# Performance work log

Measured on AMD Instinct MI355X. Metric: run time of the kernel, lower is better.

The kernel has to match this reference:

```python
import jax, jax.numpy as jnp
import numpy as np

N_HEAD = 16
N_EMBD = 1024
HEAD_DIM = N_EMBD // N_HEAD


def setup_inputs() -> dict:
    key = jax.random.key(0)
    k1, k2, k3 = jax.random.split(key, 3)
    B, T, C = 2, 2048, N_EMBD
    x = jax.random.normal(k1, (B, T, C), dtype=jnp.float32)
    # nn.Linear weights: (out_features, in_features)
    W_attn = jax.random.normal(k2, (3 * C, C), dtype=jnp.float32) * 0.02
    W_proj = jax.random.normal(k3, (C, C), dtype=jnp.float32) * 0.02
    return {"x": x, "W_attn": W_attn, "W_proj": W_proj}


def reference(x, W_attn, W_proj):
    B, T, C = x.shape
    h, hd = N_HEAD, HEAD_DIM
    # c_attn: x @ W^T, then split into q, k, v
    qkv = jnp.einsum('btc,dc->btd', x, W_attn)  # [B, T, 3C]
    q, k, v = jnp.split(qkv, 3, axis=-1)
    # [B, T, C] -> [B, h, T, hd]
    q = q.reshape(B, T, h, hd).transpose(0, 2, 1, 3)
    k = k.reshape(B, T, h, hd).transpose(0, 2, 1, 3)
    v = v.reshape(B, T, h, hd).transpose(0, 2, 1, 3)
    # NOTE: no 1/sqrt(hd) scaling in the original module
    logits = jnp.einsum('bhnk,bhmk->bhnm', q, k)  # [B, h, T, T]
    causal = jnp.tril(jnp.ones((T, T), dtype=bool))  # [T, T]
    logits = jnp.where(causal[None, None, :, :], logits, -jnp.inf)
    weights = jax.nn.softmax(logits, axis=-1)
    O = jnp.einsum('bhnm,bhmv->bhnv', weights, v)  # [B, h, T, hd]
    # Original: einsum('bhnv,hdv->bnd', O, c_proj.weight) with weight viewed as (h, d, v)
    Wp = W_proj.reshape(h, C, hd)
    Y = jnp.einsum('bhnv,hdv->bnd', O, Wp)  # [B, T, C]
    return Y
```

## Files before the change

kernel.cpp:

```cpp
#include <hip/hip_runtime.h>
#include <stdint.h>
#include <math.h>

#define B_    2
#define T_    2048
#define C_    1024
#define H_    16
#define D_    64
#define MTOT  4096
#define NQKV  3072
#define KDIM  1024

#define LOG2E 1.4426950408889634f

typedef short short8 __attribute__((ext_vector_type(8)));
typedef float f32x4  __attribute__((ext_vector_type(4)));

__device__ __forceinline__ uint16_t f2b(float f) {
    union { float f; uint32_t u; } x; x.f = f;
    uint32_t u = x.u;
    return (uint16_t)((u + 0x7FFFu + ((u >> 16) & 1u)) >> 16);
}
__device__ __forceinline__ uint32_t packb2(float a, float b) {
    union { float f; uint32_t u; } x, y; x.f = a; y.f = b;
    return ((x.u + 0x8000u) >> 16) | ((y.u + 0x8000u) & 0xffff0000u);
}
__device__ __forceinline__ uint32_t packb2_rne(float a, float b) {
    return (uint32_t)f2b(a) | ((uint32_t)f2b(b) << 16);
}
__device__ __forceinline__ float fexp2(float x) {
#if __has_builtin(__builtin_amdgcn_exp2f)
    return __builtin_amdgcn_exp2f(x);
#else
    return exp2f(x);
#endif
}

__global__ __launch_bounds__(256) void cast_all(const float* __restrict__ x,
                                                const float* __restrict__ wa,
                                                uint16_t* __restrict__ xb,
                                                uint16_t* __restrict__ wab,
                                                int n4x, int n4w) {
    int i = blockIdx.x * blockDim.x + threadIdx.x;
    const float* src; uint16_t* dst; int j;
    if (i < n4x) { src = x; dst = xb; j = i; }
    else { j = i - n4x; if (j >= n4w) return; src = wa; dst = wab; }
    float4 v = ((const float4*)src)[j];
    ushort4 o;
    o.x = f2b(v.x); o.y = f2b(v.y); o.z = f2b(v.z); o.w = f2b(v.w);
    ((ushort4*)dst)[j] = o;
}

__global__ __launch_bounds__(256) void cast_wp(const float* __restrict__ wp,
                                               uint16_t* __restrict__ wt) {
    int i = blockIdx.x * blockDim.x + threadIdx.x;
    int j4 = (i & 255) * 4;
    int d  = i >> 8;
    int h = j4 >> 6, v = j4 & 63;
    float4 val = *(const float4*)(wp + h * 65536 + d * 64 + v);
    ushort4 o;
    o.x = f2b(val.x); o.y = f2b(val.y); o.z = f2b(val.z); o.w = f2b(val.w);
    *(ushort4*)(wt + d * 1024 + j4) = o;
}

__global__ __launch_bounds__(256, 3) void gemm_qkv(const uint16_t* __restrict__ A,
                                                   const uint16_t* __restrict__ Bw,
                                                   uint16_t* __restrict__ qkvb) {
    __shared__ __align__(16) uint16_t As[128 * 64];
    __shared__ __align__(16) uint16_t Bs[128 * 64];

    int tid = threadIdx.x;
    int w = tid >> 6, lane = tid & 63;
    int qd = lane >> 4, ln = lane & 15;
    int lnx = ln & 7;
    int rowBase = blockIdx.y * 128;
    int colBase = blockIdx.x * 128;
    int mw = (w >> 1) * 64, nw = (w & 1) * 64;

    int srow = tid >> 3;
    int pchunk = tid & 7;
    int gchunk = pchunk ^ (srow & 7);

    const uint16_t* ga = A  + (size_t)(rowBase + srow) * KDIM + gchunk * 8;
    const uint16_t* gb = Bw + (size_t)(colBase + srow) * KDIM + gchunk * 8;
    uint16_t* la = &As[srow * 64 + pchunk * 8];
    uint16_t* lb = &Bs[srow * 64 + pchunk * 8];

    short8 paE[4], paO[4], pb[4];
#pragma unroll
    for (int m = 0; m < 4; m++) {
        paE[m] = *(const short8*)(ga + (size_t)m * 32 * KDIM);
        paO[m] = *(const short8*)(ga + 64 + (size_t)m * 32 * KDIM);
        pb[m]  = *(const short8*)(gb + (size_t)m * 32 * KDIM);
    }

    f32x4 acc[4][4] = {};

#define QSTEP(PAC, S)                                                            \
    {                                                                            \
        _Pragma("unroll")                                                        \
        for (int m = 0; m < 4; m++) {                                            \
            *(short8*)(la + m * 32 * 64) = PAC[m];                               \
            *(short8*)(lb + m * 32 * 64) = pb[m];                                \
        }                                                                        \
        __syncthreads();                                                         \
        if ((S) + 1 < 16) {                                                      \
            int kb_ = ((S) + 1) * 64;                                            \
            _Pragma("unroll")                                                    \
            for (int m = 0; m < 4; m++)                                          \
                pb[m] = *(const short8*)(gb + kb_ + (size_t)m * 32 * KDIM);      \
        }                                                                        \
        if ((S) + 2 < 16) {                                                      \
            int ka_ = ((S) + 2) * 64;                                            \
            _Pragma("unroll")                                                    \
            for (int m = 0; m < 4; m++)                                          \
                PAC[m] = *(const short8*)(ga + ka_ + (size_t)m * 32 * KDIM);     \
        }                                                                        \
        _Pragma("unroll")                                                        \
        for (int ks = 0; ks < 2; ks++) {                                         \
            int p = (ks * 4 + qd) ^ lnx;                                         \
            short8 a_[4], b_[4];                                                 \
            _Pragma("unroll")                                                    \
            for (int i = 0; i < 4; i++) {                                        \
                a_[i] = *(const short8*)&As[(mw + i * 16 + ln) * 64 + p * 8];    \
                b_[i] = *(const short8*)&Bs[(nw + i * 16 + ln) * 64 + p * 8];    \
            }                                                                    \
            _Pragma("unroll")                                                    \
            for (int i = 0; i < 4; i++)                                          \
                _Pragma("unroll")                                                \
                for (int j = 0; j < 4; j++)                                      \
                    acc[i][j] = __builtin_amdgcn_mfma_f32_16x16x32_bf16(a_[i], b_[j], acc[i][j], 0, 0, 0); \
        }                                                                        \
        __syncthreads();                                                         \
    }

    for (int sp = 0; sp < 8; sp++) {
        QSTEP(paE, 2 * sp);
        QSTEP(paO, 2 * sp + 1);
    }
#undef QSTEP

#pragma unroll
    for (int i = 0; i < 4; i++) {
#pragma unroll
        for (int j = 0; j < 4; j++) {
            int gcol = colBase + nw + j * 16 + ln;
            int which = gcol >> 10;
            int rem = gcol & 1023;
            int h = rem >> 6, d = rem & 63;
            if (which == 2) {
                int t0 = rowBase + mw + i * 16 + qd * 4;
                int bb = t0 >> 11, t = t0 & 2047;
                uint2 pk2;
                pk2.x = packb2_rne(acc[i][j][0], acc[i][j][1]);
                pk2.y = packb2_rne(acc[i][j][2], acc[i][j][3]);
                *(uint2*)&qkvb[(size_t)2 * 4194304 + (((size_t)(bb * H_ + h) * D_) + d) * T_ + t] = pk2;
            } else {
                float sc = (which == 0) ? LOG2E : 1.0f;
#pragma unroll
                for (int r = 0; r < 4; r++) {
                    int grow = rowBase + mw + i * 16 + qd * 4 + r;
                    int bb = grow >> 11, t = grow & 2047;
                    uint16_t val = f2b(acc[i][j][r] * sc);
                    qkvb[(size_t)which * 4194304 + (((size_t)(bb * H_ + h) * T_) + t) * D_ + d] = val;
                }
            }
        }
    }
}


#define STRIP(QS, BQ, OT, LSUM)                                              \
    if (kt * 64 <= (QS) + 15) {                                              \
        bool needm = (kt * 64 + 63 > (QS));                                  \
        f32x4 stt[4];                                                        \
        __builtin_amdgcn_s_setprio(1);                                       \
        _Pragma("unroll")                                                    \
        for (int it = 0; it < 4; it++) {                                     \
            f32x4 z = {};                                                    \
            z = __builtin_amdgcn_mfma_f32_16x16x32_bf16(ak[it][0], (BQ)[0], z, 0, 0, 0); \
            z = __builtin_amdgcn_mfma_f32_16x16x32_bf16(ak[it][1], (BQ)[1], z, 0, 0, 0); \
            stt[it] = z;                                                     \
        }                                                                    \
        __builtin_amdgcn_s_setprio(0);                                       \
        if (needm) {                                                         \
            _Pragma("unroll")                                                \
            for (int it = 0; it < 4; it++)                                   \
                _Pragma("unroll")                                            \
                for (int r = 0; r < 4; r++) {                                \
                    int t = kt * 64 + it * 16 + qd * 4 + r;                  \
                    if (t > (QS) + ln) stt[it][r] = -1.0e30f;                \
                }                                                            \
        }                                                                    \
        _Pragma("unroll")                                                    \
        for (int it = 0; it < 4; it++) {                                     \
            float p0 = fexp2(stt[it][0]);                                    \
            float p1 = fexp2(stt[it][1]);                                    \
            float p2 = fexp2(stt[it][2]);                                    \
            float p3 = fexp2(stt[it][3]);                                    \
            (LSUM) += (p0 + p1) + (p2 + p3);                                 \
            uint2 pk2;                                                       \
            pk2.x = packb2(p0, p1);                                          \
            pk2.y = packb2(p2, p3);                                          \
            *(uint2*)&Pl[w][ln][it * 16 + qd * 4] = pk2;                     \
        }                                                                    \
        short8 bp0 = *(const short8*)&Pl[w][ln][qd * 8];                     \
        short8 bp1 = *(const short8*)&Pl[w][ln][32 + qd * 8];                \
        __builtin_amdgcn_s_setprio(1);                                       \
        _Pragma("unroll")                                                    \
        for (int id = 0; id < 4; id++) {                                     \
            (OT)[id] = __builtin_amdgcn_mfma_f32_16x16x32_bf16(av[id][0], bp0, (OT)[id], 0, 0, 0); \
            (OT)[id] = __builtin_amdgcn_mfma_f32_16x16x32_bf16(av[id][1], bp1, (OT)[id], 0, 0, 0); \
        }                                                                    \
        __builtin_amdgcn_s_setprio(0);                                       \
    }

#define EPI(QS, OT, LSUM)                                                    \
    {                                                                        \
        float ssum = (LSUM);                                                 \
        ssum += __shfl_xor(ssum, 16);                                        \
        ssum += __shfl_xor(ssum, 32);                                        \
        float rl = 1.0f / ssum;                                              \
        int q = (QS) + ln;                                                   \
        _Pragma("unroll")                                                    \
        for (int id = 0; id < 4; id++) {                                     \
            float v0 = (OT)[id][0] * rl;                                     \
            float v1 = (OT)[id][1] * rl;                                     \
            float v2 = (OT)[id][2] * rl;                                     \
            float v3 = (OT)[id][3] * rl;                                     \
            uint2 pk2;                                                       \
            pk2.x = packb2_rne(v0, v1);                                      \
            pk2.y = packb2_rne(v2, v3);                                      \
            *(uint2*)&oc[(size_t)(b * T_ + q) * C_ + h * 64 + id * 16 + qd * 4] = pk2; \
        }                                                                    \
    }

__global__ __launch_bounds__(512, 2) void attn(const uint16_t* __restrict__ qkvb,
                                               uint16_t* __restrict__ oc) {
    __shared__ __align__(16) uint16_t Ks[2][64 * 64];
    __shared__ __align__(16) uint16_t Vs[2][64 * 64];
    __shared__ __align__(16) uint16_t Pl[8][16][72];

    int tid = threadIdx.x;
    int w = tid >> 6, lane = tid & 63;
    int qd = lane >> 4, ln = lane & 15;
    int lnx = ln & 7;
    int bid = blockIdx.x;
    int j = bid >> 5;
    int bh = bid & 31;
    int b = bh >> 4, h = bh & 15;

    const uint16_t* Q0 = qkvb + (size_t)bh * T_ * D_;
    const uint16_t* K  = Q0 + 4194304;
    const uint16_t* Vt = qkvb + (size_t)2 * 4194304 + (size_t)bh * D_ * T_;

    int qsA = j * 128 + w * 16;
    int qsB = (15 - j) * 128 + w * 16;
    int nt  = 32 - 2 * j;

    short8 bqA[2], bqB[2];
#pragma unroll
    for (int ks = 0; ks < 2; ks++) {
        bqA[ks] = *(const short8*)(Q0 + (size_t)(qsA + ln) * D_ + ks * 32 + qd * 8);
        bqB[ks] = *(const short8*)(Q0 + (size_t)(qsB + ln) * D_ + ks * 32 + qd * 8);
    }

    int srow = tid >> 3;
    int pch = tid & 7;
    int gch = pch ^ (srow & 7);
    const uint16_t* gk = K  + (size_t)srow * D_ + gch * 8;
    const uint16_t* gv = Vt + (size_t)srow * T_ + gch * 8;
    int lofs = srow * 64 + pch * 8;

    short8 pk = *(const short8*)gk;
    short8 pv = *(const short8*)gv;

    f32x4 otA[4] = {}, otB[4] = {};
    float lA = 0.f, lB = 0.f;

    int c = 0;
    for (int kt = 0; kt < nt; kt++) {
        *(short8*)&Ks[c][lofs] = pk;
        *(short8*)&Vs[c][lofs] = pv;
        __syncthreads();
        if (kt + 1 < nt) {
            pk = *(const short8*)(gk + (size_t)(kt + 1) * 64 * D_);
            pv = *(const short8*)(gv + (size_t)(kt + 1) * 64);
        }
        short8 ak[4][2], av[4][2];
#pragma unroll
        for (int ks = 0; ks < 2; ks++) {
            int p8 = ((ks * 4 + qd) ^ lnx) * 8;
#pragma unroll
            for (int it = 0; it < 4; it++) {
                ak[it][ks] = *(const short8*)&Ks[c][(it * 16 + ln) * 64 + p8];
                av[it][ks] = *(const short8*)&Vs[c][(it * 16 + ln) * 64 + p8];
            }
        }
        STRIP(qsA, bqA, otA, lA);
        STRIP(qsB, bqB, otB, lB);
        c ^= 1;
    }

    EPI(qsA, otA, lA);
    EPI(qsB, otB, lB);
}

__global__ __launch_bounds__(256, 3) void gemm_out(const uint16_t* __restrict__ A,
                                                   const uint16_t* __restrict__ Bw,
                                                   float* __restrict__ out) {
    __shared__ __align__(16) uint16_t As[128 * 64];
    __shared__ __align__(16) uint16_t Bs[64 * 64];

    int tid = threadIdx.x;
    int w = tid >> 6, lane = tid & 63;
    int qd = lane >> 4, ln = lane & 15;
    int lnx = ln & 7;
    int rowBase = blockIdx.y * 128;
    int colBase = blockIdx.x * 64;
    int mw = (w >> 1) * 64, nw = (w & 1) * 32;

    int srow = tid >> 3;
    int pchunk = tid & 7;
    int gchunk = pchunk ^ (srow & 7);

    const uint16_t* ga = A  + (size_t)(rowBase + srow) * KDIM + gchunk * 8;
    const uint16_t* gb = Bw + (size_t)(colBase + srow) * KDIM + gchunk * 8;
    uint16_t* la = &As[srow * 64 + pchunk * 8];
    uint16_t* lb = &Bs[srow * 64 + pchunk * 8];

    short8 paE[4], paO[4], pb[2];
#pragma unroll
    for (int m = 0; m < 4; m++) {
        paE[m] = *(const short8*)(ga + (size_t)m * 32 * KDIM);
        paO[m] = *(const short8*)(ga + 64 + (size_t)m * 32 * KDIM);
    }
#pragma unroll
    for (int m = 0; m < 2; m++)
        pb[m] = *(const short8*)(gb + (size_t)m * 32 * KDIM);

    f32x4 acc[4][2] = {};

#define OSTEP(PAC, S)                                                            \
    {                                                                            \
        _Pragma("unroll")                                                        \
        for (int m = 0; m < 4; m++)                                              \
            *(short8*)(la + m * 32 * 64) = PAC[m];                               \
        _Pragma("unroll")                                                        \
        for (int m = 0; m < 2; m++)                                              \
            *(short8*)(lb + m * 32 * 64) = pb[m];                                \
        __syncthreads();                                                         \
        if ((S) + 1 < 16) {                                                      \
            int kb_ = ((S) + 1) * 64;                                            \
            _Pragma("unroll")                                                    \
            for (int m = 0; m < 2; m++)                                          \
                pb[m] = *(const short8*)(gb + kb_ + (size_t)m * 32 * KDIM);      \
        }                                                                        \
        if ((S) + 2 < 16) {                                                      \
            int ka_ = ((S) + 2) * 64;                                            \
            _Pragma("unroll")                                                    \
            for (int m = 0; m < 4; m++)                                          \
                PAC[m] = *(const short8*)(ga + ka_ + (size_t)m * 32 * KDIM);     \
        }                                                                        \
        _Pragma("unroll")                                                        \
        for (int ks = 0; ks < 2; ks++) {                                         \
            int p = (ks * 4 + qd) ^ lnx;                                         \
            short8 a_[4], b_[2];                                                 \
            _Pragma("unroll")                                                    \
            for (int i = 0; i < 4; i++)                                          \
                a_[i] = *(const short8*)&As[(mw + i * 16 + ln) * 64 + p * 8];    \
            _Pragma("unroll")                                                    \
            for (int j = 0; j < 2; j++)                                          \
                b_[j] = *(const short8*)&Bs[(nw + j * 16 + ln) * 64 + p * 8];    \
            _Pragma("unroll")                                                    \
            for (int i = 0; i < 4; i++)                                          \
                _Pragma("unroll")                                                \
                for (int j = 0; j < 2; j++)                                      \
                    acc[i][j] = __builtin_amdgcn_mfma_f32_16x16x32_bf16(a_[i], b_[j], acc[i][j], 0, 0, 0); \
        }                                                                        \
        __syncthreads();                                                         \
    }

    for (int sp = 0; sp < 8; sp++) {
        OSTEP(paE, 2 * sp);
        OSTEP(paO, 2 * sp + 1);
    }
#undef OSTEP

#pragma unroll
    for (int i = 0; i < 4; i++)
#pragma unroll
        for (int j = 0; j < 2; j++)
#pragma unroll
            for (int r = 0; r < 4; r++) {
                int grow = rowBase + mw + i * 16 + qd * 4 + r;
                int gcol = colBase + nw + j * 16 + ln;
                out[(size_t)grow * 1024 + gcol] = acc[i][j][r];
            }
}

extern "C" void kernel_launch(void* const* d_in, const int* in_sizes, int n_in,
                              void* d_out, int out_size, void* d_ws, size_t ws_size,
                              hipStream_t stream) {
    const float* x  = (const float*)d_in[0];
    const float* Wa = (const float*)d_in[1];
    const float* Wp = (const float*)d_in[2];
    float* out = (float*)d_out;

    uint16_t* ws   = (uint16_t*)d_ws;
    uint16_t* xb   = ws;
    uint16_t* Wab  = xb + 4194304;
    uint16_t* Wtb  = Wab + 3145728;
    uint16_t* qkvb = Wtb + 1048576;
    uint16_t* ob   = qkvb + (size_t)3 * 4194304;

    cast_all<<<7168, 256, 0, stream>>>(x, Wa, xb, Wab, 4194304 / 4, 3145728 / 4);
    cast_wp<<<1024, 256, 0, stream>>>(Wp, Wtb);
    gemm_qkv<<<dim3(24, 32), 256, 0, stream>>>(xb, Wab, qkvb);
    attn<<<256, 512, 0, stream>>>(qkvb, ob);
    gemm_out<<<dim3(16, 32), 256, 0, stream>>>(ob, Wtb, out);
}
```

Before: 164.1 us.

## Merge weight casts and split QKV GEMM into Q/K and V kernels

Folds the W_proj transpose-cast into the main cast kernel, which removes one launch. The QKV GEMM becomes two kernels. For Q/K the MFMA operands are swapped so each lane holds four consecutive head-dim values and can write packed 8-byte stores instead of scalar 2-byte scattered stores. The V kernel keeps the transposed packed store. The cost is one extra launch, a smaller grid per GEMM, and duplicated code.

```diff
diff --git a/kernel.cpp b/kernel.cpp
--- a/kernel.cpp
+++ b/kernel.cpp
@@ -36,36 +36,40 @@
 #endif
 }
 
+#define N4X 1048576
+#define N4W 786432
+#define N4P 262144
+
 __global__ __launch_bounds__(256) void cast_all(const float* __restrict__ x,
                                                 const float* __restrict__ wa,
+                                                const float* __restrict__ wp,
                                                 uint16_t* __restrict__ xb,
                                                 uint16_t* __restrict__ wab,
-                                                int n4x, int n4w) {
+                                                uint16_t* __restrict__ wt) {
     int i = blockIdx.x * blockDim.x + threadIdx.x;
-    const float* src; uint16_t* dst; int j;
-    if (i < n4x) { src = x; dst = xb; j = i; }
-    else { j = i - n4x; if (j >= n4w) return; src = wa; dst = wab; }
-    float4 v = ((const float4*)src)[j];
-    ushort4 o;
-    o.x = f2b(v.x); o.y = f2b(v.y); o.z = f2b(v.z); o.w = f2b(v.w);
-    ((ushort4*)dst)[j] = o;
-}
-
-__global__ __launch_bounds__(256) void cast_wp(const float* __restrict__ wp,
-                                               uint16_t* __restrict__ wt) {
-    int i = blockIdx.x * blockDim.x + threadIdx.x;
-    int j4 = (i & 255) * 4;
-    int d  = i >> 8;
-    int h = j4 >> 6, v = j4 & 63;
-    float4 val = *(const float4*)(wp + h * 65536 + d * 64 + v);
-    ushort4 o;
-    o.x = f2b(val.x); o.y = f2b(val.y); o.z = f2b(val.z); o.w = f2b(val.w);
-    *(ushort4*)(wt + d * 1024 + j4) = o;
-}
-
-__global__ __launch_bounds__(256, 3) void gemm_qkv(const uint16_t* __restrict__ A,
-                                                   const uint16_t* __restrict__ Bw,
-                                                   uint16_t* __restrict__ qkvb) {
+    if (i < N4X + N4W) {
+        const float* src; uint16_t* dst; int j;
+        if (i < N4X) { src = x; dst = xb; j = i; }
+        else { src = wa; dst = wab; j = i - N4X; }
+        float4 v = ((const float4*)src)[j];
+        ushort4 o;
+        o.x = f2b(v.x); o.y = f2b(v.y); o.z = f2b(v.z); o.w = f2b(v.w);
+        ((ushort4*)dst)[j] = o;
+    } else {
+        int j = i - (N4X + N4W);
+        int j4 = (j & 255) * 4;
+        int d  = j >> 8;
+        int h = j4 >> 6, v = j4 & 63;
+        float4 val = *(const float4*)(wp + h * 65536 + d * 64 + v);
+        ushort4 o;
+        o.x = f2b(val.x); o.y = f2b(val.y); o.z = f2b(val.z); o.w = f2b(val.w);
+        *(ushort4*)(wt + d * 1024 + j4) = o;
+    }
+}
+
+__global__ __launch_bounds__(256, 3) void gemm_qkv_qk(const uint16_t* __restrict__ A,
+                                                      const uint16_t* __restrict__ Bw,
+                                                      uint16_t* __restrict__ qkvb) {
     __shared__ __align__(16) uint16_t As[128 * 64];
     __shared__ __align__(16) uint16_t Bs[128 * 64];
 
@@ -129,7 +133,7 @@
             for (int i = 0; i < 4; i++)                                          \
                 _Pragma("unroll")                                                \
                 for (int j = 0; j < 4; j++)                                      \
-                    acc[i][j] = __builtin_amdgcn_mfma_f32_16x16x32_bf16(a_[i], b_[j], acc[i][j], 0, 0, 0); \
+                    acc[i][j] = __builtin_amdgcn_mfma_f32_16x16x32_bf16(b_[j], a_[i], acc[i][j], 0, 0, 0); \
         }                                                                        \
         __syncthreads();                                                         \
     }
@@ -140,31 +144,115 @@
     }
 #undef QSTEP
 
+    int which = (colBase + nw) >> 10;
+    float sc = (which == 0) ? LOG2E : 1.0f;
+#pragma unroll
+    for (int i = 0; i < 4; i++) {
+#pragma unroll
+        for (int j = 0; j < 4; j++) {
+            int mcol = colBase + nw + j * 16 + qd * 4;
+            int rem = mcol & 1023;
+            int h = rem >> 6, d0 = rem & 63;
+            int grow = rowBase + mw + i * 16 + ln;
+            int bb = grow >> 11, tt = grow & 2047;
+            uint2 pk2;
+            pk2.x = packb2_rne(acc[i][j][0] * sc, acc[i][j][1] * sc);
+            pk2.y = packb2_rne(acc[i][j][2] * sc, acc[i][j][3] * sc);
+            *(uint2*)&qkvb[(size_t)which * 4194304 + ((size_t)(bb * H_ + h) * T_ + tt) * D_ + d0] = pk2;
+        }
+    }
+}
+
+__global__ __launch_bounds__(256, 3) void gemm_qkv_v(const uint16_t* __restrict__ A,
+                                                     const uint16_t* __restrict__ Bw,
+                                                     uint16_t* __restrict__ qkvb) {
+    __shared__ __align__(16) uint16_t As[128 * 64];
+    __shared__ __align__(16) uint16_t Bs[128 * 64];
+
+    int tid = threadIdx.x;
+    int w = tid >> 6, lane = tid & 63;
+    int qd = lane >> 4, ln = lane & 15;
+    int lnx = ln & 7;
+    int rowBase = blockIdx.y * 128;
+    int colBase = 2048 + blockIdx.x * 128;
+    int mw = (w >> 1) * 64, nw = (w & 1) * 64;
+
+    int srow = tid >> 3;
+    int pchunk = tid & 7;
+    int gchunk = pchunk ^ (srow & 7);
+
+    const uint16_t* ga = A  + (size_t)(rowBase + srow) * KDIM + gchunk * 8;
+    const uint16_t* gb = Bw + (size_t)(colBase + srow) * KDIM + gchunk * 8;
+    uint16_t* la = &As[srow * 64 + pchunk * 8];
+    uint16_t* lb = &Bs[srow * 64 + pchunk * 8];
+
+    short8 paE[4], paO[4], pb[4];
+#pragma unroll
+    for (int m = 0; m < 4; m++) {
+        paE[m] = *(const short8*)(ga + (size_t)m * 32 * KDIM);
+        paO[m] = *(const short8*)(ga + 64 + (size_t)m * 32 * KDIM);
+        pb[m]  = *(const short8*)(gb + (size_t)m * 32 * KDIM);
+    }
+
+    f32x4 acc[4][4] = {};
+
+#define VSTEP(PAC, S)                                                            \
+    {                                                                            \
+        _Pragma("unroll")                                                        \
+        for (int m = 0; m < 4; m++) {                                            \
+            *(short8*)(la + m * 32 * 64) = PAC[m];                               \
+            *(short8*)(lb + m * 32 * 64) = pb[m];                                \
+        }                                                                        \
+        __syncthreads();                                                         \
+        if ((S) + 1 < 16) {                                                      \
+            int kb_ = ((S) + 1) * 64;                                            \
+            _Pragma("unroll")                                                    \
+            for (int m = 0; m < 4; m++)                                          \
+                pb[m] = *(const short8*)(gb + kb_ + (size_t)m * 32 * KDIM);      \
+        }                                                                        \
+        if ((S) + 2 < 16) {                                                      \
+            int ka_ = ((S) + 2) * 64;                                            \
+            _Pragma("unroll")                                                    \
+            for (int m = 0; m < 4; m++)                                          \
+                PAC[m] = *(const short8*)(ga + ka_ + (size_t)m * 32 * KDIM);     \
+        }                                                                        \
+        _Pragma("unroll")                                                        \
+        for (int ks = 0; ks < 2; ks++) {                                         \
+            int p = (ks * 4 + qd) ^ lnx;                                         \
+            short8 a_[4], b_[4];                                                 \
+            _Pragma("unroll")                                                    \
+            for (int i = 0; i < 4; i++) {                                        \
+                a_[i] = *(const short8*)&As[(mw + i * 16 + ln) * 64 + p * 8];    \
+                b_[i] = *(const short8*)&Bs[(nw + i * 16 + ln) * 64 + p * 8];    \
+            }                                                                    \
+            _Pragma("unroll")                                                    \
+            for (int i = 0; i < 4; i++)                                          \
+                _Pragma("unroll")                                                \
+                for (int j = 0; j < 4; j++)                                      \
+                    acc[i][j] = __builtin_amdgcn_mfma_f32_16x16x32_bf16(a_[i], b_[j], acc[i][j], 0, 0, 0); \
+        }                                                                        \
+        __syncthreads();                                                         \
+    }
+
+    for (int sp = 0; sp < 8; sp++) {
+        VSTEP(paE, 2 * sp);
+        VSTEP(paO, 2 * sp + 1);
+    }
+#undef VSTEP
+
 #pragma unroll
     for (int i = 0; i < 4; i++) {
 #pragma unroll
         for (int j = 0; j < 4; j++) {
             int gcol = colBase + nw + j * 16 + ln;
-            int which = gcol >> 10;
             int rem = gcol & 1023;
             int h = rem >> 6, d = rem & 63;
-            if (which == 2) {
-                int t0 = rowBase + mw + i * 16 + qd * 4;
-                int bb = t0 >> 11, t = t0 & 2047;
-                uint2 pk2;
-                pk2.x = packb2_rne(acc[i][j][0], acc[i][j][1]);
-                pk2.y = packb2_rne(acc[i][j][2], acc[i][j][3]);
-                *(uint2*)&qkvb[(size_t)2 * 4194304 + (((size_t)(bb * H_ + h) * D_) + d) * T_ + t] = pk2;
-            } else {
-                float sc = (which == 0) ? LOG2E : 1.0f;
-#pragma unroll
-                for (int r = 0; r < 4; r++) {
-                    int grow = rowBase + mw + i * 16 + qd * 4 + r;
-                    int bb = grow >> 11, t = grow & 2047;
-                    uint16_t val = f2b(acc[i][j][r] * sc);
-                    qkvb[(size_t)which * 4194304 + (((size_t)(bb * H_ + h) * T_) + t) * D_ + d] = val;
-                }
-            }
+            int t0 = rowBase + mw + i * 16 + qd * 4;
+            int bb = t0 >> 11, t = t0 & 2047;
+            uint2 pk2;
+            pk2.x = packb2_rne(acc[i][j][0], acc[i][j][1]);
+            pk2.y = packb2_rne(acc[i][j][2], acc[i][j][3]);
+            *(uint2*)&qkvb[(size_t)2 * 4194304 + (((size_t)(bb * H_ + h) * D_) + d) * T_ + t] = pk2;
         }
     }
 }
@@ -414,9 +502,9 @@
     uint16_t* qkvb = Wtb + 1048576;
     uint16_t* ob   = qkvb + (size_t)3 * 4194304;
 
-    cast_all<<<7168, 256, 0, stream>>>(x, Wa, xb, Wab, 4194304 / 4, 3145728 / 4);
-    cast_wp<<<1024, 256, 0, stream>>>(Wp, Wtb);
-    gemm_qkv<<<dim3(24, 32), 256, 0, stream>>>(xb, Wab, qkvb);
+    cast_all<<<8192, 256, 0, stream>>>(x, Wa, Wp, xb, Wab, Wtb);
+    gemm_qkv_qk<<<dim3(16, 32), 256, 0, stream>>>(xb, Wab, qkvb);
+    gemm_qkv_v<<<dim3(8, 32), 256, 0, stream>>>(xb, Wab, qkvb);
     attn<<<256, 512, 0, stream>>>(qkvb, ob);
     gemm_out<<<dim3(16, 32), 256, 0, stream>>>(ob, Wtb, out);
 }
```

Result: slower. 172.2 us (+4.9%).
